# Optimization experiments

Measured on AMD Instinct MI355X. Metric: run time of the kernel, lower is better.

Reference implementation:

```python
import jax, jax.numpy as jnp
import numpy as np

N = 100000   # num nodes
D = 128      # node_emb_dim
R = 8        # num_relations
E = 1600000  # num edges


def setup_inputs() -> dict:
    key = jax.random.key(0)
    k0, k1, k2, k3, k4 = jax.random.split(key, 5)
    x = jax.random.normal(k0, (N, D), dtype=jnp.float32)
    edge_index = jax.random.randint(k1, (2, E), 0, N, dtype=jnp.int32)
    edge_type = jax.random.randint(k2, (E,), 0, R, dtype=jnp.int32)
    scale = 1.0 / np.sqrt(D)
    W = (jax.random.normal(k3, (R, D, D), dtype=jnp.float32) * scale)       # per-relation weight
    W_root = (jax.random.normal(k4, (D, D), dtype=jnp.float32) * scale)     # root (self-loop) weight
    bias = jnp.zeros((D,), dtype=jnp.float32)
    return {"x": x, "W": W, "W_root": W_root, "bias": bias,
            "edge_index": edge_index, "edge_type": edge_type}


def reference(x, W, W_root, bias, edge_index, edge_type):
    # PyG RGCNConv (num_bases=None, aggr='mean', root_weight=True, bias=True):
    # out_i = x_i @ W_root + bias + sum_r mean_{j in N_r(i)} x_j @ W_r
    # Mean aggregation is linear, so aggregate neighbor features per (node, relation)
    # first, then apply the per-relation transform (avoids [E,D,D] intermediates).
    src, dst = edge_index[0], edge_index[1]
    seg = dst * R + edge_type                                   # [E] segment id per (dst, rel)
    cnt = jax.ops.segment_sum(jnp.ones((E,), x.dtype), seg, num_segments=N * R)  # [N*R]
    sums = jax.ops.segment_sum(x[src], seg, num_segments=N * R)                   # [N*R, D]
    mean = sums / jnp.maximum(cnt, 1.0)[:, None]                                  # [N*R, D]
    rel_out = jnp.einsum('nrd,rde->ne', mean.reshape(N, R, D), W)                 # [N, D]
    return rel_out + x @ W_root + bias
```

## Files before the change

kernel.cpp:

```cpp
#include <hip/hip_runtime.h>


constexpr int D = 128;
constexpr int R = 8;
constexpr int TILE = 2048;

typedef __bf16 bf16x8 __attribute__((ext_vector_type(8)));
typedef float  f32x4  __attribute__((ext_vector_type(4)));
typedef unsigned short u16x8 __attribute__((ext_vector_type(8)));
typedef unsigned short u16x4 __attribute__((ext_vector_type(4)));

__device__ __forceinline__ unsigned short f2bf(float f) {
    unsigned u = __builtin_bit_cast(unsigned, f);
    u += 0x7FFFu + ((u >> 16) & 1u);
    return (unsigned short)(u >> 16);
}

__global__ __launch_bounds__(256)
void xbf_kernel(const float* __restrict__ x, unsigned short* __restrict__ xbf, int nquad) {
    int stride = gridDim.x * 256;
    for (int i = blockIdx.x * 256 + threadIdx.x; i < nquad; i += stride) {
        float4 v = ((const float4*)x)[i];
        u16x4 o;
        o[0] = f2bf(v.x); o[1] = f2bf(v.y); o[2] = f2bf(v.z); o[3] = f2bf(v.w);
        ((u16x4*)xbf)[i] = o;
    }
}

__global__ __launch_bounds__(256)
void bcount_kernel(const int* __restrict__ dst, const int* __restrict__ et,
                   int* __restrict__ meta, int E) {
    __shared__ int cnt8[8];
    if (threadIdx.x < 8) cnt8[threadIdx.x] = 0;
    __syncthreads();
    int stride = gridDim.x * 256;
    for (int e = blockIdx.x * 256 + threadIdx.x; e < E; e += stride) {
        int seg = dst[e] * R + et[e];
        atomicAdd(&cnt8[(seg >> 7) & 7], 1);
    }
    __syncthreads();
    if (threadIdx.x < 8) atomicAdd(&meta[threadIdx.x], cnt8[threadIdx.x]);
}

__global__ void bscan_kernel(int* __restrict__ meta) {
    if (threadIdx.x == 0) {
        int cum = 0;
        for (int p = 0; p < 8; ++p) {
            meta[8 + p]  = cum;
            meta[16 + p] = cum;
            cum += meta[p];
        }
    }
}

__global__ __launch_bounds__(256)
void bucketA_kernel(const int* __restrict__ src, const int* __restrict__ dst,
                    const int* __restrict__ et, int* __restrict__ ebuf_seg,
                    int* __restrict__ ebuf_src, int* __restrict__ meta, int E) {
    __shared__ int cntw[4][8];
    __shared__ int basew[4][8];
    const int tid = threadIdx.x;
    const int w   = tid >> 6;
    for (int t0 = blockIdx.x * TILE; t0 < E; t0 += gridDim.x * TILE) {
        if (tid < 32) cntw[tid >> 3][tid & 7] = 0;
        __syncthreads();
        int seg[8], sr[8], pt[8];
        bool ok[8];
        #pragma unroll
        for (int j = 0; j < 8; ++j) {
            int e = t0 + j * 256 + tid;
            ok[j] = e < E;
            if (ok[j]) {
                seg[j] = dst[e] * R + et[e];
                sr[j]  = src[e];
                pt[j]  = (seg[j] >> 7) & 7;
                atomicAdd(&cntw[w][pt[j]], 1);
            }
        }
        __syncthreads();
        if (tid < 8) {
            int p = tid;
            int tot = cntw[0][p] + cntw[1][p] + cntw[2][p] + cntw[3][p];
            int b = atomicAdd(&meta[16 + p], tot);
            basew[0][p] = b;               b += cntw[0][p];
            basew[1][p] = b;               b += cntw[1][p];
            basew[2][p] = b;               b += cntw[2][p];
            basew[3][p] = b;
            cntw[0][p] = 0; cntw[1][p] = 0; cntw[2][p] = 0; cntw[3][p] = 0;
        }
        __syncthreads();
        #pragma unroll
        for (int j = 0; j < 8; ++j) {
            if (ok[j]) {
                int r   = atomicAdd(&cntw[w][pt[j]], 1);
                int pos = basew[w][pt[j]] + r;
                ebuf_seg[pos] = seg[j];
                ebuf_src[pos] = sr[j];
            }
        }
        __syncthreads();
    }
}

__global__ __launch_bounds__(256)
void hist_kernel(const int* __restrict__ ebuf_seg, const int* __restrict__ meta,
                 int* __restrict__ hist) {
    int part = blockIdx.x & 7;
    int nb   = gridDim.x >> 3;
    int lo   = meta[8 + part];
    int n    = meta[part];
    for (int i = (blockIdx.x >> 3) * 256 + threadIdx.x; i < n; i += nb * 256)
        atomicAdd(&hist[ebuf_seg[lo + i]], 1);
}

__global__ __launch_bounds__(256)
void block_sums_kernel(const int* __restrict__ hs, int* __restrict__ bsum, int n) {
    __shared__ int sh[256];
    int i = blockIdx.x * 256 + threadIdx.x;
    sh[threadIdx.x] = (i < n) ? hs[i] : 0;
    __syncthreads();
    for (int off = 128; off > 0; off >>= 1) {
        if (threadIdx.x < off) sh[threadIdx.x] += sh[threadIdx.x + off];
        __syncthreads();
    }
    if (threadIdx.x == 0) bsum[blockIdx.x] = sh[0];
}

__global__ __launch_bounds__(64)
void scan_bsum_kernel(int* __restrict__ bsum, int nb) {
    int lane = threadIdx.x;
    int carry = 0;
    for (int base = 0; base < nb; base += 64) {
        int i = base + lane;
        int orig = (i < nb) ? bsum[i] : 0;
        int v = orig;
        #pragma unroll
        for (int off = 1; off < 64; off <<= 1) {
            int u = __shfl_up(v, off, 64);
            if (lane >= off) v += u;
        }
        int tot = __shfl(v, 63, 64);
        if (i < nb) bsum[i] = carry + (v - orig);
        carry += tot;
    }
}

__global__ __launch_bounds__(256)
void scan_block_kernel(int* __restrict__ hs, const int* __restrict__ bsum,
                       int* __restrict__ cursor, int n, int E) {
    __shared__ int sh[256];
    int tid = threadIdx.x;
    int i = blockIdx.x * 256 + tid;
    int v = (i < n) ? hs[i] : 0;
    sh[tid] = v;
    __syncthreads();
    for (int off = 1; off < 256; off <<= 1) {
        int u = (tid >= off) ? sh[tid - off] : 0;
        __syncthreads();
        sh[tid] += u;
        __syncthreads();
    }
    int st = bsum[blockIdx.x] + sh[tid] - v;
    if (i < n) { hs[i] = st; cursor[i] = st; }
    if (i == n) hs[n] = E;
}

__global__ __launch_bounds__(256)
void bucketB_kernel(const int* __restrict__ ebuf_seg, const int* __restrict__ ebuf_src,
                    const int* __restrict__ meta, int* __restrict__ cursor,
                    int* __restrict__ spack) {
    int part = blockIdx.x & 7;
    int nb   = gridDim.x >> 3;
    int lo   = meta[8 + part];
    int n    = meta[part];
    for (int i = (blockIdx.x >> 3) * 256 + threadIdx.x; i < n; i += nb * 256) {
        int seg = ebuf_seg[lo + i];
        int s   = ebuf_src[lo + i];
        int pos = atomicAdd(&cursor[seg], 1);
        spack[pos] = s;
    }
}

__global__ __launch_bounds__(256)
void aggregate_kernel(const unsigned short* __restrict__ xbf,
                      const int* __restrict__ spack,
                      const int* __restrict__ hstart,
                      unsigned short* __restrict__ mean,
                      int nseg, int tshift, int c0) {
    int idx = blockIdx.x * 256 + threadIdx.x;
    int seg = idx >> tshift;
    int c8  = idx & ((1 << tshift) - 1);
    if (seg >= nseg) return;
    int p0 = hstart[seg], p1 = hstart[seg + 1];
    int coff = c0 + c8 * 8;
    float a[8] = {};
    for (int p = p0; p < p1; ++p) {
        int s = spack[p];
        u16x8 v = *(const u16x8*)(xbf + ((size_t)s << 7) + coff);
        #pragma unroll
        for (int j = 0; j < 8; ++j)
            a[j] += __builtin_bit_cast(float, (unsigned)v[j] << 16);
    }
    float inv = (p1 > p0) ? 1.0f / (float)(p1 - p0) : 0.0f;
    u16x8 o;
    #pragma unroll
    for (int j = 0; j < 8; ++j) o[j] = f2bf(a[j] * inv);
    __builtin_nontemporal_store(o, (u16x8*)(mean + ((size_t)seg << (tshift + 3)) + c8 * 8));
}

__global__ __launch_bounds__(256)
void wallt_kernel(const float* __restrict__ Wroot, const float* __restrict__ W,
                  unsigned short* __restrict__ WallTc, int KW, int CW, int c0, int first) {
    int idx = blockIdx.x * 256 + threadIdx.x;
    if (idx >= 128 * KW) return;
    int n = idx / KW, kk = idx % KW;
    float v;
    if (first && kk < 128) {
        v = Wroot[kk * 128 + n];
    } else {
        int lk = kk - (first ? 128 : 0);
        int r = lk / CW, cc = lk % CW;
        v = W[((size_t)r * 128 + c0 + cc) * 128 + n];
    }
    WallTc[idx] = f2bf(v);
}

template<bool FIRST>
__global__ __launch_bounds__(256)
void mfma_gemm_kernel(const unsigned short* __restrict__ xbf,
                      const unsigned short* __restrict__ mean,
                      const unsigned short* __restrict__ WallTc,
                      const float* __restrict__ bias,
                      float* __restrict__ out,
                      int N, int NT, int KW, int MROW) {
    __shared__ unsigned short As[128][32];
    __shared__ unsigned short Bs[128][32];
    const int tid  = threadIdx.x;
    const int row0 = blockIdx.x * 128;
    const int lane = tid & 63;
    const int wid  = tid >> 6;
    const int wm   = wid >> 1;
    const int wn   = wid & 1;
    const int srow = tid >> 1;
    const int sh16 = (tid & 1) * 16;

    f32x4 acc[4][4] = {};

    const int  node = row0 + srow;
    const bool nok  = node < N;

    for (int kt = 0; kt < NT; ++kt) {
        if (kt) __syncthreads();
        u16x8 a0, a1;
        #pragma unroll
        for (int j = 0; j < 8; ++j) { a0[j] = 0; a1[j] = 0; }
        if (FIRST && kt < 4) {
            if (nok) {
                const u16x8* xp = (const u16x8*)(xbf + ((size_t)node << 7) + kt * 32 + sh16);
                a0 = xp[0]; a1 = xp[1];
            }
        } else {
            if (nok) {
                const u16x8* mp = (const u16x8*)(mean + (size_t)node * MROW
                                                 + (kt - (FIRST ? 4 : 0)) * 32 + sh16);
                a0 = mp[0]; a1 = mp[1];
            }
        }
        const u16x8* wp = (const u16x8*)(WallTc + (size_t)srow * KW + kt * 32 + sh16);
        u16x8 b0 = wp[0], b1 = wp[1];

        *(u16x8*)&As[srow][sh16]     = a0;
        *(u16x8*)&As[srow][sh16 + 8] = a1;
        *(u16x8*)&Bs[srow][sh16]     = b0;
        *(u16x8*)&Bs[srow][sh16 + 8] = b1;
        __syncthreads();

        const int kg = (lane >> 4) * 8;
        const int rl = lane & 15;
        bf16x8 av[4], bv[4];
        #pragma unroll
        for (int f = 0; f < 4; ++f) {
            av[f] = __builtin_bit_cast(bf16x8, *(const u16x8*)&As[wm * 64 + f * 16 + rl][kg]);
            bv[f] = __builtin_bit_cast(bf16x8, *(const u16x8*)&Bs[wn * 64 + f * 16 + rl][kg]);
        }
        #pragma unroll
        for (int mf = 0; mf < 4; ++mf)
            #pragma unroll
            for (int nf = 0; nf < 4; ++nf)
                acc[mf][nf] = __builtin_amdgcn_mfma_f32_16x16x32_bf16(av[mf], bv[nf],
                                                                     acc[mf][nf], 0, 0, 0);
    }

    const int rl = lane & 15;
    const int rg = lane >> 4;
    #pragma unroll
    for (int nf = 0; nf < 4; ++nf) {
        int n = wn * 64 + nf * 16 + rl;
        float bb = FIRST ? bias[n] : 0.0f;
        #pragma unroll
        for (int mf = 0; mf < 4; ++mf) {
            #pragma unroll
            for (int i = 0; i < 4; ++i) {
                int nd = row0 + wm * 64 + mf * 16 + rg * 4 + i;
                if (nd < N) {
                    size_t o = (size_t)nd * 128 + n;
                    if (FIRST) out[o] = acc[mf][nf][i] + bb;
                    else       out[o] += acc[mf][nf][i];
                }
            }
        }
    }
}

extern "C" void kernel_launch(void* const* d_in, const int* in_sizes, int n_in,
                              void* d_out, int out_size, void* d_ws, size_t ws_size,
                              hipStream_t stream) {
    const float* x     = (const float*)d_in[0];
    const float* W     = (const float*)d_in[1];
    const float* Wroot = (const float*)d_in[2];
    const float* bias  = (const float*)d_in[3];
    const int*   ei    = (const int*)d_in[4];
    const int*   et    = (const int*)d_in[5];
    float*       out   = (float*)d_out;

    const int N = in_sizes[0] / D;
    const int E = in_sizes[5];
    const int* src = ei;
    const int* dst = ei + E;

    const int NSEG = N * R;
    const int NB   = (NSEG + 256) / 256;

    const size_t xbf_bytes    = (size_t)N * D * 2;
    const size_t walltc_bytes = (size_t)128 * 1152 * 2;
    const size_t fixed_bytes  = xbf_bytes + walltc_bytes +
                                ((size_t)(NSEG + 1) + NSEG + E + NB + 32) * 4 + 256;

    int CW = 0, tshift = 0;
    const int cands[3]   = {128, 64, 32};
    const int tshifts[3] = {4, 3, 2};
    for (int i = 0; i < 3; ++i) {
        size_t need = (size_t)NSEG * cands[i] * 2 + fixed_bytes;
        if (need <= ws_size) { CW = cands[i]; tshift = tshifts[i]; break; }
    }
    if (CW == 0) return;

    char* p = (char*)d_ws;
    unsigned short* mean   = (unsigned short*)p;  p += (size_t)NSEG * CW * 2;
    unsigned short* xbf    = (unsigned short*)p;  p += xbf_bytes;
    unsigned short* WallTc = (unsigned short*)p;  p += walltc_bytes;
    int* hstart = (int*)p;  p += (size_t)(NSEG + 1) * 4;
    int* cursor = (int*)p;  p += (size_t)NSEG * 4;
    int* spack  = (int*)p;  p += (size_t)E * 4;
    int* bsum   = (int*)p;  p += (size_t)NB * 4;
    int* meta   = (int*)p;

    int* ebuf_seg = (int*)mean;
    int* ebuf_src = ebuf_seg + E;

    hipMemsetAsync(hstart, 0, (size_t)(NSEG + 1) * 4, stream);
    hipMemsetAsync(meta, 0, 32 * 4, stream);

    xbf_kernel<<<2048, 256, 0, stream>>>(x, xbf, N * D / 4);

    bcount_kernel<<<1024, 256, 0, stream>>>(dst, et, meta, E);
    bscan_kernel<<<1, 64, 0, stream>>>(meta);
    bucketA_kernel<<<(E + TILE - 1) / TILE, 256, 0, stream>>>(
        src, dst, et, ebuf_seg, ebuf_src, meta, E);
    hist_kernel<<<768, 256, 0, stream>>>(ebuf_seg, meta, hstart);
    block_sums_kernel<<<NB, 256, 0, stream>>>(hstart, bsum, NSEG);
    scan_bsum_kernel<<<1, 64, 0, stream>>>(bsum, NB);
    scan_block_kernel<<<NB, 256, 0, stream>>>(hstart, bsum, cursor, NSEG, E);
    bucketB_kernel<<<768, 256, 0, stream>>>(ebuf_seg, ebuf_src, meta, cursor, spack);

    const int gx  = (N + 127) / 128;
    const int nch = D / CW;
    for (int c = 0; c < nch; ++c) {
        int c0    = c * CW;
        int first = (c == 0);
        long long aggth = (long long)NSEG << tshift;
        aggregate_kernel<<<(int)((aggth + 255) / 256), 256, 0, stream>>>(
            xbf, spack, hstart, mean, NSEG, tshift, c0);
        int KW   = (first ? 128 : 0) + R * CW;
        int NT   = KW / 32;
        int MROW = R * CW;
        wallt_kernel<<<(128 * KW + 255) / 256, 256, 0, stream>>>(
            Wroot, W, WallTc, KW, CW, c0, first);
        if (first)
            mfma_gemm_kernel<true><<<gx, 256, 0, stream>>>(
                xbf, mean, WallTc, bias, out, N, NT, KW, MROW);
        else
            mfma_gemm_kernel<false><<<gx, 256, 0, stream>>>(
                xbf, mean, WallTc, bias, out, N, NT, KW, MROW);
    }
}
```

Before: 435.7 us.

## Fuse neighbor aggregation with relation GEMM in one per-node-block kernel

Replaces the separate aggregate and GEMM launches with one kernel per 128-node block. Each block gathers mean features for four relations at a time into a per-node slab, then runs the MFMA GEMM over that slab, and finishes with the root-weight term. The weight transpose now covers all relations and the root in a single launch up front, and the gather loop is unrolled by four for more loads in flight. The intent is to keep the mean data hot in cache and cut launches and out read-modify-write passes. The cost is far fewer concurrent threads doing the latency-bound gather, with aggregation and compute serialized inside each block.

```diff
diff --git a/kernel.cpp b/kernel.cpp
--- a/kernel.cpp
+++ b/kernel.cpp
@@ -14,6 +14,9 @@
     unsigned u = __builtin_bit_cast(unsigned, f);
     u += 0x7FFFu + ((u >> 16) & 1u);
     return (unsigned short)(u >> 16);
+}
+__device__ __forceinline__ float bf2f(unsigned short h) {
+    return __builtin_bit_cast(float, (unsigned)h << 16);
 }
 
 __global__ __launch_bounds__(256)
@@ -182,93 +185,133 @@
 }
 
 __global__ __launch_bounds__(256)
-void aggregate_kernel(const unsigned short* __restrict__ xbf,
-                      const int* __restrict__ spack,
-                      const int* __restrict__ hstart,
-                      unsigned short* __restrict__ mean,
-                      int nseg, int tshift, int c0) {
+void wallt_kernel(const float* __restrict__ Wroot, const float* __restrict__ W,
+                  unsigned short* __restrict__ WallTc) {
     int idx = blockIdx.x * 256 + threadIdx.x;
-    int seg = idx >> tshift;
-    int c8  = idx & ((1 << tshift) - 1);
-    if (seg >= nseg) return;
-    int p0 = hstart[seg], p1 = hstart[seg + 1];
-    int coff = c0 + c8 * 8;
-    float a[8] = {};
-    for (int p = p0; p < p1; ++p) {
-        int s = spack[p];
-        u16x8 v = *(const u16x8*)(xbf + ((size_t)s << 7) + coff);
-        #pragma unroll
-        for (int j = 0; j < 8; ++j)
-            a[j] += __builtin_bit_cast(float, (unsigned)v[j] << 16);
-    }
-    float inv = (p1 > p0) ? 1.0f / (float)(p1 - p0) : 0.0f;
-    u16x8 o;
-    #pragma unroll
-    for (int j = 0; j < 8; ++j) o[j] = f2bf(a[j] * inv);
-    __builtin_nontemporal_store(o, (u16x8*)(mean + ((size_t)seg << (tshift + 3)) + c8 * 8));
-}
-
-__global__ __launch_bounds__(256)
-void wallt_kernel(const float* __restrict__ Wroot, const float* __restrict__ W,
-                  unsigned short* __restrict__ WallTc, int KW, int CW, int c0, int first) {
-    int idx = blockIdx.x * 256 + threadIdx.x;
-    if (idx >= 128 * KW) return;
-    int n = idx / KW, kk = idx % KW;
-    float v;
-    if (first && kk < 128) {
-        v = Wroot[kk * 128 + n];
-    } else {
-        int lk = kk - (first ? 128 : 0);
-        int r = lk / CW, cc = lk % CW;
-        v = W[((size_t)r * 128 + c0 + cc) * 128 + n];
-    }
+    if (idx >= 128 * 1152) return;
+    int n = idx / 1152, k = idx % 1152;
+    float v = (k < 1024) ? W[(size_t)(k >> 7) * 16384 + (size_t)(k & 127) * 128 + n]
+                         : Wroot[(size_t)(k - 1024) * 128 + n];
     WallTc[idx] = f2bf(v);
 }
 
-template<bool FIRST>
-__global__ __launch_bounds__(256)
-void mfma_gemm_kernel(const unsigned short* __restrict__ xbf,
-                      const unsigned short* __restrict__ mean,
-                      const unsigned short* __restrict__ WallTc,
-                      const float* __restrict__ bias,
-                      float* __restrict__ out,
-                      int N, int NT, int KW, int MROW) {
+__global__ __launch_bounds__(256)
+void fused_kernel(const unsigned short* __restrict__ xbf,
+                  const unsigned short* __restrict__ WallTc,
+                  const int* __restrict__ spack,
+                  const int* __restrict__ hstart,
+                  unsigned short* __restrict__ meanslab,
+                  const float* __restrict__ bias,
+                  float* __restrict__ out, int N) {
     __shared__ unsigned short As[128][32];
     __shared__ unsigned short Bs[128][32];
     const int tid  = threadIdx.x;
-    const int row0 = blockIdx.x * 128;
+    const int nd0  = blockIdx.x * 128;
     const int lane = tid & 63;
     const int wid  = tid >> 6;
-    const int wm   = wid >> 1;
-    const int wn   = wid & 1;
+    const int wm   = wid >> 1, wn = wid & 1;
     const int srow = tid >> 1;
     const int sh16 = (tid & 1) * 16;
+    const int gnode = nd0 + srow;
+    const bool nok  = gnode < N;
 
     f32x4 acc[4][4] = {};
 
-    const int  node = row0 + srow;
-    const bool nok  = node < N;
-
-    for (int kt = 0; kt < NT; ++kt) {
-        if (kt) __syncthreads();
+    for (int g = 0; g < 2; ++g) {
+        if (g) __syncthreads();
+
+        for (int i = 0; i < 32; ++i) {
+            int t  = i * 256 + tid;
+            int c8 = t & 15;
+            int rl = (t >> 4) & 3;
+            int nl = t >> 6;
+            int node = nd0 + nl;
+            if (node < N) {
+                int seg = node * R + g * 4 + rl;
+                int p0 = hstart[seg], p1 = hstart[seg + 1];
+                int coff = c8 * 8;
+                float a[8] = {};
+                for (int p = p0; p < p1; p += 4) {
+                    int s0 = spack[p];
+                    int s1 = (p + 1 < p1) ? spack[p + 1] : -1;
+                    int s2 = (p + 2 < p1) ? spack[p + 2] : -1;
+                    int s3 = (p + 3 < p1) ? spack[p + 3] : -1;
+                    u16x8 v0 = *(const u16x8*)(xbf + ((size_t)s0 << 7) + coff);
+                    #pragma unroll
+                    for (int j = 0; j < 8; ++j) a[j] += bf2f(v0[j]);
+                    if (s1 >= 0) {
+                        u16x8 v = *(const u16x8*)(xbf + ((size_t)s1 << 7) + coff);
+                        #pragma unroll
+                        for (int j = 0; j < 8; ++j) a[j] += bf2f(v[j]);
+                    }
+                    if (s2 >= 0) {
+                        u16x8 v = *(const u16x8*)(xbf + ((size_t)s2 << 7) + coff);
+                        #pragma unroll
+                        for (int j = 0; j < 8; ++j) a[j] += bf2f(v[j]);
+                    }
+                    if (s3 >= 0) {
+                        u16x8 v = *(const u16x8*)(xbf + ((size_t)s3 << 7) + coff);
+                        #pragma unroll
+                        for (int j = 0; j < 8; ++j) a[j] += bf2f(v[j]);
+                    }
+                }
+                float inv = (p1 > p0) ? 1.0f / (float)(p1 - p0) : 0.0f;
+                u16x8 o;
+                #pragma unroll
+                for (int j = 0; j < 8; ++j) o[j] = f2bf(a[j] * inv);
+                *(u16x8*)(meanslab + ((size_t)node << 9) + rl * 128 + coff) = o;
+            }
+        }
+        __syncthreads();
+
+        for (int kt = 0; kt < 16; ++kt) {
+            if (kt) __syncthreads();
+            u16x8 a0, a1;
+            #pragma unroll
+            for (int j = 0; j < 8; ++j) { a0[j] = 0; a1[j] = 0; }
+            if (nok) {
+                const u16x8* mp = (const u16x8*)(meanslab + ((size_t)gnode << 9)
+                                                 + kt * 32 + sh16);
+                a0 = mp[0]; a1 = mp[1];
+            }
+            const u16x8* wp = (const u16x8*)(WallTc + (size_t)srow * 1152
+                                             + g * 512 + kt * 32 + sh16);
+            u16x8 b0 = wp[0], b1 = wp[1];
+            *(u16x8*)&As[srow][sh16]     = a0;
+            *(u16x8*)&As[srow][sh16 + 8] = a1;
+            *(u16x8*)&Bs[srow][sh16]     = b0;
+            *(u16x8*)&Bs[srow][sh16 + 8] = b1;
+            __syncthreads();
+
+            const int kg = (lane >> 4) * 8;
+            const int rl2 = lane & 15;
+            bf16x8 av[4], bv[4];
+            #pragma unroll
+            for (int f = 0; f < 4; ++f) {
+                av[f] = __builtin_bit_cast(bf16x8, *(const u16x8*)&As[wm * 64 + f * 16 + rl2][kg]);
+                bv[f] = __builtin_bit_cast(bf16x8, *(const u16x8*)&Bs[wn * 64 + f * 16 + rl2][kg]);
+            }
+            #pragma unroll
+            for (int mf = 0; mf < 4; ++mf)
+                #pragma unroll
+                for (int nf = 0; nf < 4; ++nf)
+                    acc[mf][nf] = __builtin_amdgcn_mfma_f32_16x16x32_bf16(av[mf], bv[nf],
+                                                                         acc[mf][nf], 0, 0, 0);
+        }
+    }
+
+    for (int kt = 0; kt < 4; ++kt) {
+        __syncthreads();
         u16x8 a0, a1;
         #pragma unroll
         for (int j = 0; j < 8; ++j) { a0[j] = 0; a1[j] = 0; }
-        if (FIRST && kt < 4) {
-            if (nok) {
-                const u16x8* xp = (const u16x8*)(xbf + ((size_t)node << 7) + kt * 32 + sh16);
-                a0 = xp[0]; a1 = xp[1];
-            }
-        } else {
-            if (nok) {
-                const u16x8* mp = (const u16x8*)(mean + (size_t)node * MROW
-                                                 + (kt - (FIRST ? 4 : 0)) * 32 + sh16);
-                a0 = mp[0]; a1 = mp[1];
-            }
-        }
-        const u16x8* wp = (const u16x8*)(WallTc + (size_t)srow * KW + kt * 32 + sh16);
+        if (nok) {
+            const u16x8* xp = (const u16x8*)(xbf + ((size_t)gnode << 7) + kt * 32 + sh16);
+            a0 = xp[0]; a1 = xp[1];
+        }
+        const u16x8* wp = (const u16x8*)(WallTc + (size_t)srow * 1152
+                                         + 1024 + kt * 32 + sh16);
         u16x8 b0 = wp[0], b1 = wp[1];
-
         *(u16x8*)&As[srow][sh16]     = a0;
         *(u16x8*)&As[srow][sh16 + 8] = a1;
         *(u16x8*)&Bs[srow][sh16]     = b0;
@@ -276,12 +319,12 @@
         __syncthreads();
 
         const int kg = (lane >> 4) * 8;
-        const int rl = lane & 15;
+        const int rl2 = lane & 15;
         bf16x8 av[4], bv[4];
         #pragma unroll
         for (int f = 0; f < 4; ++f) {
-            av[f] = __builtin_bit_cast(bf16x8, *(const u16x8*)&As[wm * 64 + f * 16 + rl][kg]);
-            bv[f] = __builtin_bit_cast(bf16x8, *(const u16x8*)&Bs[wn * 64 + f * 16 + rl][kg]);
+            av[f] = __builtin_bit_cast(bf16x8, *(const u16x8*)&As[wm * 64 + f * 16 + rl2][kg]);
+            bv[f] = __builtin_bit_cast(bf16x8, *(const u16x8*)&Bs[wn * 64 + f * 16 + rl2][kg]);
         }
         #pragma unroll
         for (int mf = 0; mf < 4; ++mf)
@@ -291,22 +334,18 @@
                                                                      acc[mf][nf], 0, 0, 0);
     }
 
-    const int rl = lane & 15;
-    const int rg = lane >> 4;
+    const int rl2 = lane & 15;
+    const int rg  = lane >> 4;
     #pragma unroll
     for (int nf = 0; nf < 4; ++nf) {
-        int n = wn * 64 + nf * 16 + rl;
-        float bb = FIRST ? bias[n] : 0.0f;
+        int n = wn * 64 + nf * 16 + rl2;
+        float bb = bias[n];
         #pragma unroll
         for (int mf = 0; mf < 4; ++mf) {
             #pragma unroll
             for (int i = 0; i < 4; ++i) {
-                int nd = row0 + wm * 64 + mf * 16 + rg * 4 + i;
-                if (nd < N) {
-                    size_t o = (size_t)nd * 128 + n;
-                    if (FIRST) out[o] = acc[mf][nf][i] + bb;
-                    else       out[o] += acc[mf][nf][i];
-                }
+                int nd = nd0 + wm * 64 + mf * 16 + rg * 4 + i;
+                if (nd < N) out[(size_t)nd * D + n] = acc[mf][nf][i] + bb;
             }
         }
     }
@@ -331,37 +370,31 @@
     const int NSEG = N * R;
     const int NB   = (NSEG + 256) / 256;
 
+    const size_t slab_bytes   = (size_t)N * 512 * 2;
     const size_t xbf_bytes    = (size_t)N * D * 2;
     const size_t walltc_bytes = (size_t)128 * 1152 * 2;
-    const size_t fixed_bytes  = xbf_bytes + walltc_bytes +
-                                ((size_t)(NSEG + 1) + NSEG + E + NB + 32) * 4 + 256;
-
-    int CW = 0, tshift = 0;
-    const int cands[3]   = {128, 64, 32};
-    const int tshifts[3] = {4, 3, 2};
-    for (int i = 0; i < 3; ++i) {
-        size_t need = (size_t)NSEG * cands[i] * 2 + fixed_bytes;
-        if (need <= ws_size) { CW = cands[i]; tshift = tshifts[i]; break; }
-    }
-    if (CW == 0) return;
+    const size_t need = slab_bytes + xbf_bytes + walltc_bytes +
+                        ((size_t)(NSEG + 1) + NSEG + E + NB + 32) * 4 + 256;
+    if (ws_size < need) return;
 
     char* p = (char*)d_ws;
-    unsigned short* mean   = (unsigned short*)p;  p += (size_t)NSEG * CW * 2;
-    unsigned short* xbf    = (unsigned short*)p;  p += xbf_bytes;
-    unsigned short* WallTc = (unsigned short*)p;  p += walltc_bytes;
+    unsigned short* meanslab = (unsigned short*)p;  p += slab_bytes;
+    unsigned short* xbf      = (unsigned short*)p;  p += xbf_bytes;
+    unsigned short* WallTc   = (unsigned short*)p;  p += walltc_bytes;
     int* hstart = (int*)p;  p += (size_t)(NSEG + 1) * 4;
     int* cursor = (int*)p;  p += (size_t)NSEG * 4;
     int* spack  = (int*)p;  p += (size_t)E * 4;
     int* bsum   = (int*)p;  p += (size_t)NB * 4;
     int* meta   = (int*)p;
 
-    int* ebuf_seg = (int*)mean;
+    int* ebuf_seg = (int*)meanslab;
     int* ebuf_src = ebuf_seg + E;
 
     hipMemsetAsync(hstart, 0, (size_t)(NSEG + 1) * 4, stream);
     hipMemsetAsync(meta, 0, 32 * 4, stream);
 
     xbf_kernel<<<2048, 256, 0, stream>>>(x, xbf, N * D / 4);
+    wallt_kernel<<<(128 * 1152 + 255) / 256, 256, 0, stream>>>(Wroot, W, WallTc);
 
     bcount_kernel<<<1024, 256, 0, stream>>>(dst, et, meta, E);
     bscan_kernel<<<1, 64, 0, stream>>>(meta);
@@ -373,24 +406,7 @@
     scan_block_kernel<<<NB, 256, 0, stream>>>(hstart, bsum, cursor, NSEG, E);
     bucketB_kernel<<<768, 256, 0, stream>>>(ebuf_seg, ebuf_src, meta, cursor, spack);
 
-    const int gx  = (N + 127) / 128;
-    const int nch = D / CW;
-    for (int c = 0; c < nch; ++c) {
-        int c0    = c * CW;
-        int first = (c == 0);
-        long long aggth = (long long)NSEG << tshift;
-        aggregate_kernel<<<(int)((aggth + 255) / 256), 256, 0, stream>>>(
-            xbf, spack, hstart, mean, NSEG, tshift, c0);
-        int KW   = (first ? 128 : 0) + R * CW;
-        int NT   = KW / 32;
-        int MROW = R * CW;
-        wallt_kernel<<<(128 * KW + 255) / 256, 256, 0, stream>>>(
-            Wroot, W, WallTc, KW, CW, c0, first);
-        if (first)
-            mfma_gemm_kernel<true><<<gx, 256, 0, stream>>>(
-                xbf, mean, WallTc, bias, out, N, NT, KW, MROW);
-        else
-            mfma_gemm_kernel<false><<<gx, 256, 0, stream>>>(
-                xbf, mean, WallTc, bias, out, N, NT, KW, MROW);
-    }
-}
+    const int gx = (N + 127) / 128;
+    fused_kernel<<<gx, 256, 0, stream>>>(xbf, WallTc, spack, hstart, meanslab,
+                                         bias, out, N);
+}
```

Measured after the change: 567.9 us. +30.3%, slower.
